# Kernel optimization log

Hardware: AMD Instinct MI355X
Metric: run time of the kernel (lower is better)

## Reference

```python
import jax, jax.numpy as jnp
import numpy as np

B, S, D, H = 4, 2048, 1024, 16
HD = D // H  # head dim = 64


def setup_inputs() -> dict:
    key = jax.random.key(0)
    ks = jax.random.split(key, 8)
    s = 1.0 / np.sqrt(D)
    return {
        "query": jax.random.normal(ks[0], (B, S, D), jnp.float32),
        "key": jax.random.normal(ks[1], (B, S, D), jnp.float32),
        "value": jax.random.normal(ks[2], (B, S, D), jnp.float32),
        "wq": jax.random.normal(ks[3], (D, D), jnp.float32) * s,
        "wk": jax.random.normal(ks[4], (D, D), jnp.float32) * s,
        "wv": jax.random.normal(ks[5], (D, D), jnp.float32) * s,
        "wo": jax.random.normal(ks[6], (D, D), jnp.float32) * s,
        "bo": jax.random.normal(ks[7], (D,), jnp.float32) * s,
    }


def reference(query, key, value, wq, wk, wv, wo, bo):
    # project and split heads: [B,S,D] -> [B,H,S,HD]
    def split_heads(x, w):
        return (x @ w.T).reshape(B, S, H, HD).transpose(0, 2, 1, 3)

    q = split_heads(query, wq)
    k = split_heads(key, wk)
    v = split_heads(value, wv)
    scores = jnp.einsum('bhqd,bhkd->bhqk', q, k) / jnp.sqrt(jnp.float32(HD))
    attn = jax.nn.softmax(scores, axis=-1)
    out = jnp.einsum('bhqk,bhkd->bhqd', attn, v)
    out = out.transpose(0, 2, 1, 3).reshape(B, S, D)
    return out @ wo.T + bo
```

## Files before the change

kernel.cpp:

```cpp
#include <hip/hip_runtime.h>
#include <stdint.h>


#define NSEQ 2048
#define NDIM 1024
#define NE   8388608

typedef unsigned short u16;
typedef unsigned int   u32;
typedef __bf16 bf16x8 __attribute__((ext_vector_type(8)));
typedef float  f32x4  __attribute__((ext_vector_type(4)));

__device__ __forceinline__ u16 f2bf(float f) {
  return (u16)((__builtin_bit_cast(u32, f) + 0x8000u) >> 16);
}
__device__ __forceinline__ u32 pack_bf2(float lo, float hi) {
  u32 a = __builtin_bit_cast(u32, lo) + 0x8000u;
  u32 b = __builtin_bit_cast(u32, hi) + 0x8000u;
  return __builtin_amdgcn_perm(b, a, 0x07060302);
}

__device__ __forceinline__ void async_load16(const u16* gsrc, u16* ldst) {
  __builtin_amdgcn_global_load_lds(
      (const __attribute__((address_space(1))) void*)gsrc,
      (__attribute__((address_space(3))) void*)ldst, 16, 0, 0);
}

__device__ __forceinline__ void conv_body(const float* __restrict__ src,
                                          u16* __restrict__ dst, int blk) {
  const int i = blk * 256 + (int)threadIdx.x;
  const float4 a = ((const float4*)src)[2 * i];
  const float4 b = ((const float4*)src)[2 * i + 1];
  uint4 o;
  o.x = pack_bf2(a.x, a.y); o.y = pack_bf2(a.z, a.w);
  o.z = pack_bf2(b.x, b.y); o.w = pack_bf2(b.z, b.w);
  ((uint4*)dst)[i] = o;
}
__global__ __launch_bounds__(256) void conv_big_kernel(
    const float* __restrict__ query, const float* __restrict__ keyi,
    const float* __restrict__ value, u16* __restrict__ Xq,
    u16* __restrict__ Xk, u16* __restrict__ Xv) {
  int blk = blockIdx.x;
  const float* src; u16* dst;
  if (blk < 4096)      { src = query; dst = Xq; }
  else if (blk < 8192) { src = keyi;  dst = Xk; blk -= 4096; }
  else                 { src = value; dst = Xv; blk -= 8192; }
  conv_body(src, dst, blk);
}
__global__ __launch_bounds__(256) void conv_w_kernel(
    const float* __restrict__ wq, const float* __restrict__ wk,
    const float* __restrict__ wv, const float* __restrict__ wo,
    u16* __restrict__ Wall) {
  int blk = blockIdx.x;
  const int z = blk >> 9;
  blk &= 511;
  const float* src = (z == 0) ? wq : (z == 1) ? wk : (z == 2) ? wv : wo;
  conv_body(src, Wall + (size_t)z * 1048576, blk);
}

template <bool OUTF32, bool BIAS>
__device__ __forceinline__ void gemm_core(const u16* __restrict__ A,
                                          const u16* __restrict__ B,
                                          void* __restrict__ Yv,
                                          const float* __restrict__ bias,
                                          float scale, long m0, long n0,
                                          long ldy) {
  __shared__ u16 At[128 * 32];
  __shared__ u16 Bt[128 * 32];
  const int t    = threadIdx.x;
  const int lane = t & 63;
  const int w    = t >> 6;
  const int m    = lane & 15;
  const int q    = lane >> 4;
  const int wr   = w >> 1;
  const int wc   = w & 1;
  const int srow = t >> 2;
  const int scol = (t & 3) * 8;

  f32x4 acc[4][4];
#pragma unroll
  for (int i = 0; i < 4; i++)
#pragma unroll
    for (int j = 0; j < 4; j++) acc[i][j] = (f32x4){0.f, 0.f, 0.f, 0.f};

  for (int k0 = 0; k0 < NDIM; k0 += 32) {
    __syncthreads();
    async_load16(A + (m0 + srow) * NDIM + k0 + scol, At + w * 512);
    async_load16(A + (m0 + 64 + srow) * NDIM + k0 + scol, At + 2048 + w * 512);
    async_load16(B + (n0 + srow) * NDIM + k0 + scol, Bt + w * 512);
    async_load16(B + (n0 + 64 + srow) * NDIM + k0 + scol, Bt + 2048 + w * 512);
    __syncthreads();

    bf16x8 a[4], b[4];
#pragma unroll
    for (int mi = 0; mi < 4; mi++)
      a[mi] = *(const bf16x8*)(At + (wr * 64 + mi * 16 + m) * 32 + q * 8);
#pragma unroll
    for (int ni = 0; ni < 4; ni++)
      b[ni] = *(const bf16x8*)(Bt + (wc * 64 + ni * 16 + m) * 32 + q * 8);
#pragma unroll
    for (int mi = 0; mi < 4; mi++)
#pragma unroll
      for (int ni = 0; ni < 4; ni++)
        acc[mi][ni] = __builtin_amdgcn_mfma_f32_16x16x32_bf16(a[mi], b[ni], acc[mi][ni], 0, 0, 0);
  }

#pragma unroll
  for (int mi = 0; mi < 4; mi++) {
#pragma unroll
    for (int ni = 0; ni < 4; ni++) {
      const long row0 = m0 + wr * 64 + mi * 16 + q * 4;
      const long col  = n0 + wc * 64 + ni * 16 + m;
      float badd = 0.f;
      if (BIAS) badd = bias[col];
#pragma unroll
      for (int r = 0; r < 4; r++) {
        const float v = acc[mi][ni][r] * scale + badd;
        if (OUTF32) ((float*)Yv)[(row0 + r) * ldy + col] = v;
        else        ((u16*)Yv)[(row0 + r) * ldy + col] = f2bf(v);
      }
    }
  }
}

__global__ __launch_bounds__(256) void gemm_qkv_kernel(
    const u16* __restrict__ Xq, const u16* __restrict__ Xk,
    const u16* __restrict__ Xv, const u16* __restrict__ Wall,
    u16* __restrict__ Qp, u16* __restrict__ Kp, u16* __restrict__ Vt) {
  const int z = blockIdx.z;
  if (z < 2) {
    const u16* A = z ? Xk : Xq;
    const u16* B = Wall + (size_t)z * 1048576;
    u16* Y       = z ? Kp : Qp;
    gemm_core<false, false>(A, B, Y, nullptr, z ? 1.0f : 0.18033688f,
                            (long)blockIdx.x * 128, (long)blockIdx.y * 128, NDIM);
  } else {
    const int flat = blockIdx.y * 64 + blockIdx.x;
    const long b   = flat >> 7;
    const int rem  = flat & 127;
    gemm_core<false, false>(Wall + 2 * 1048576, Xv + b * NSEQ * NDIM,
                            Vt + b * (long)NDIM * NSEQ, nullptr, 1.0f,
                            (long)(rem >> 4) * 128, (long)(rem & 15) * 128, NSEQ);
  }
}

__global__ __launch_bounds__(256) void gemm_out_kernel(
    const u16* __restrict__ A, const u16* __restrict__ Wall,
    float* __restrict__ Y, const float* __restrict__ bias) {
  gemm_core<true, true>(A, Wall + 3 * 1048576, Y, bias, 1.0f,
                        (long)blockIdx.x * 128, (long)blockIdx.y * 128, NDIM);
}

__global__ __launch_bounds__(256) void attn_kernel(
    const u16* __restrict__ Qp, const u16* __restrict__ Kp,
    const u16* __restrict__ Vtg, u16* __restrict__ Op) {
  __shared__ u16 Kt[64 * 72];
  __shared__ u16 Vt[64 * 72];
  __shared__ u16 Pt[4 * 32 * 72];
  const int t    = threadIdx.x;
  const int lane = t & 63;
  const int w    = t >> 6;
  const int m    = lane & 15;
  const int q    = lane >> 4;
  const int bh   = blockIdx.y;
  const int b    = bh >> 4;
  const int h    = bh & 15;
  const int wq0  = blockIdx.x * 128 + w * 32;
  const long base_bh = (long)b * NSEQ * NDIM + h * 64;
  const long vbase   = (long)b * NDIM * NSEQ + (long)(h * 64) * NSEQ;

  bf16x8 qf[2][2];
#pragma unroll
  for (int qi = 0; qi < 2; qi++)
#pragma unroll
    for (int ks = 0; ks < 2; ks++)
      qf[qi][ks] = *(const bf16x8*)(Qp + base_bh + (long)(wq0 + qi * 16 + m) * NDIM + ks * 32 + q * 8);

  f32x4 ot[2][4];
#pragma unroll
  for (int qi = 0; qi < 2; qi++)
#pragma unroll
    for (int mb = 0; mb < 4; mb++) ot[qi][mb] = (f32x4){0.f, 0.f, 0.f, 0.f};
  float lp[2] = {0.f, 0.f};

  const int srow = t >> 3;
  const int scol = (t & 7) * 8;
  u16* pt = Pt + w * (32 * 72);

  const u16* kgp = Kp + base_bh + (long)srow * NDIM + scol;
  const u16* vgp = Vtg + vbase + (long)srow * NSEQ + scol;

  int4 kr0 = *(const int4*)(kgp);
  int4 kr1 = *(const int4*)(kgp + 32l * NDIM);
  int4 vr0 = *(const int4*)(vgp);
  int4 vr1 = *(const int4*)(vgp + 32l * NSEQ);

  for (int kt = 0; kt < NSEQ / 64; kt++) {
    __syncthreads();
    *(int4*)(Kt + srow * 72 + scol)        = kr0;
    *(int4*)(Kt + (srow + 32) * 72 + scol) = kr1;
    *(int4*)(Vt + srow * 72 + scol)        = vr0;
    *(int4*)(Vt + (srow + 32) * 72 + scol) = vr1;
    __syncthreads();

    if (kt < NSEQ / 64 - 1) {
      const long k1 = (long)(kt + 1) * 64;
      kr0 = *(const int4*)(kgp + k1 * NDIM);
      kr1 = *(const int4*)(kgp + (k1 + 32) * NDIM);
      vr0 = *(const int4*)(vgp + k1);
      vr1 = *(const int4*)(vgp + 32l * NSEQ + k1);
    }

    f32x4 st[2][4];
#pragma unroll
    for (int qi = 0; qi < 2; qi++)
#pragma unroll
      for (int nb = 0; nb < 4; nb++) st[qi][nb] = (f32x4){0.f, 0.f, 0.f, 0.f};
    __builtin_amdgcn_s_setprio(1);
#pragma unroll
    for (int ks = 0; ks < 2; ks++) {
#pragma unroll
      for (int nb = 0; nb < 4; nb++) {
        bf16x8 kf = *(const bf16x8*)(Kt + (nb * 16 + m) * 72 + ks * 32 + q * 8);
        st[0][nb] = __builtin_amdgcn_mfma_f32_16x16x32_bf16(kf, qf[0][ks], st[0][nb], 0, 0, 0);
        st[1][nb] = __builtin_amdgcn_mfma_f32_16x16x32_bf16(kf, qf[1][ks], st[1][nb], 0, 0, 0);
      }
    }
    __builtin_amdgcn_s_setprio(0);

#pragma unroll
    for (int qi = 0; qi < 2; qi++)
#pragma unroll
      for (int nb = 0; nb < 4; nb++) {
        const float p0 = __builtin_amdgcn_exp2f(st[qi][nb][0]);
        const float p1 = __builtin_amdgcn_exp2f(st[qi][nb][1]);
        const float p2 = __builtin_amdgcn_exp2f(st[qi][nb][2]);
        const float p3 = __builtin_amdgcn_exp2f(st[qi][nb][3]);
        lp[qi] += (p0 + p1) + (p2 + p3);
        uint2 pk;
        pk.x = pack_bf2(p0, p1);
        pk.y = pack_bf2(p2, p3);
        *(uint2*)(pt + (qi * 16 + m) * 72 + nb * 16 + q * 4) = pk;
      }

    __builtin_amdgcn_s_setprio(1);
#pragma unroll
    for (int ks2 = 0; ks2 < 2; ks2++) {
      bf16x8 pf[2];
#pragma unroll
      for (int qi = 0; qi < 2; qi++)
        pf[qi] = *(const bf16x8*)(pt + (qi * 16 + m) * 72 + ks2 * 32 + q * 8);
#pragma unroll
      for (int mb = 0; mb < 4; mb++) {
        bf16x8 vf = *(const bf16x8*)(Vt + (mb * 16 + m) * 72 + ks2 * 32 + q * 8);
        ot[0][mb] = __builtin_amdgcn_mfma_f32_16x16x32_bf16(vf, pf[0], ot[0][mb], 0, 0, 0);
        ot[1][mb] = __builtin_amdgcn_mfma_f32_16x16x32_bf16(vf, pf[1], ot[1][mb], 0, 0, 0);
      }
    }
    __builtin_amdgcn_s_setprio(0);
  }

  float rinv[2];
#pragma unroll
  for (int qi = 0; qi < 2; qi++) {
    float v = lp[qi];
    v += __shfl_xor(v, 16);
    v += __shfl_xor(v, 32);
    rinv[qi] = 1.0f / v;
  }

#pragma unroll
  for (int qi = 0; qi < 2; qi++) {
#pragma unroll
    for (int mb = 0; mb < 4; mb++) {
      uint2 pk;
      pk.x = pack_bf2(ot[qi][mb][0] * rinv[qi], ot[qi][mb][1] * rinv[qi]);
      pk.y = pack_bf2(ot[qi][mb][2] * rinv[qi], ot[qi][mb][3] * rinv[qi]);
      *(uint2*)(pt + m * 72 + mb * 16 + q * 4) = pk;
    }
#pragma unroll
    for (int c = 0; c < 2; c++) {
      const int u   = c * 64 + lane;
      const int qr  = u >> 3;
      const int oct = u & 7;
      const int4 val = *(const int4*)(pt + qr * 72 + oct * 8);
      const long s   = wq0 + qi * 16 + qr;
      *(int4*)(Op + base_bh + s * NDIM + oct * 8) = val;
    }
  }
}

extern "C" void kernel_launch(void* const* d_in, const int* in_sizes, int n_in,
                              void* d_out, int out_size, void* d_ws, size_t ws_size,
                              hipStream_t stream) {
  const float* query = (const float*)d_in[0];
  const float* keyi  = (const float*)d_in[1];
  const float* value = (const float*)d_in[2];
  const float* wq    = (const float*)d_in[3];
  const float* wk    = (const float*)d_in[4];
  const float* wv    = (const float*)d_in[5];
  const float* wo    = (const float*)d_in[6];
  const float* bo    = (const float*)d_in[7];

  u16* ws = (u16*)d_ws;
  u16* Qp = ws;
  u16* Kp = ws + (size_t)NE;
  u16* Vt = ws + 2 * (size_t)NE;
  u16* XqO = ws + 3 * (size_t)NE;

  u16* Xk = (u16*)d_out;
  u16* Xv = (u16*)d_out + (size_t)NE;
  u16* Wall = (u16*)d_in[0];

  dim3 blk(256, 1, 1);
  conv_big_kernel<<<dim3(12288, 1, 1), blk, 0, stream>>>(query, keyi, value, XqO, Xk, Xv);
  conv_w_kernel<<<dim3(2048, 1, 1), blk, 0, stream>>>(wq, wk, wv, wo, Wall);
  gemm_qkv_kernel<<<dim3(64, 8, 3), blk, 0, stream>>>(XqO, Xk, Xv, Wall, Qp, Kp, Vt);
  attn_kernel<<<dim3(16, 64, 1), blk, 0, stream>>>(Qp, Kp, Vt, XqO);
  gemm_out_kernel<<<dim3(64, 8, 1), blk, 0, stream>>>(XqO, Wall, (float*)d_out, bo);
}
```

Before: 349.8 us.

## Keep softmax probabilities in registers by permuting V tile layout in LDS

The exp'd score fragments are packed directly into the B-operand registers of the PV MFMA instead of being written to and re-read from a per-wave LDS P buffer. To make that register layout line up, V columns are scattered into LDS with a permuted key ordering. The P shared buffer is removed, the epilogue reuses the K tile storage behind an extra barrier, and launch bounds request 4 blocks per CU to raise occupancy. The main risks are the correctness of the permutation and register pressure under the new launch bound.

```diff
diff --git a/kernel.cpp b/kernel.cpp
--- a/kernel.cpp
+++ b/kernel.cpp
@@ -151,12 +151,11 @@
                         (long)blockIdx.x * 128, (long)blockIdx.y * 128, NDIM);
 }
 
-__global__ __launch_bounds__(256) void attn_kernel(
+__global__ __launch_bounds__(256, 4) void attn_kernel(
     const u16* __restrict__ Qp, const u16* __restrict__ Kp,
     const u16* __restrict__ Vtg, u16* __restrict__ Op) {
   __shared__ u16 Kt[64 * 72];
   __shared__ u16 Vt[64 * 72];
-  __shared__ u16 Pt[4 * 32 * 72];
   const int t    = threadIdx.x;
   const int lane = t & 63;
   const int w    = t >> 6;
@@ -184,8 +183,13 @@
   float lp[2] = {0.f, 0.f};
 
   const int srow = t >> 3;
-  const int scol = (t & 7) * 8;
-  u16* pt = Pt + w * (32 * 72);
+  const int c8   = t & 7;
+  const int scol = c8 * 8;
+
+  const int vnb   = c8 >> 1;
+  const int vbase_c = 32 * (vnb >> 1) + 4 * (vnb & 1);
+  const int vcol0 = vbase_c + 8 * ((2 * c8) & 3);
+  const int vcol1 = vbase_c + 8 * ((2 * c8 + 1) & 3);
 
   const u16* kgp = Kp + base_bh + (long)srow * NDIM + scol;
   const u16* vgp = Vtg + vbase + (long)srow * NSEQ + scol;
@@ -195,12 +199,16 @@
   int4 vr0 = *(const int4*)(vgp);
   int4 vr1 = *(const int4*)(vgp + 32l * NSEQ);
 
+  const f32x4 zz = (f32x4){0.f, 0.f, 0.f, 0.f};
+
   for (int kt = 0; kt < NSEQ / 64; kt++) {
     __syncthreads();
     *(int4*)(Kt + srow * 72 + scol)        = kr0;
     *(int4*)(Kt + (srow + 32) * 72 + scol) = kr1;
-    *(int4*)(Vt + srow * 72 + scol)        = vr0;
-    *(int4*)(Vt + (srow + 32) * 72 + scol) = vr1;
+    *(uint2*)(Vt + srow * 72 + vcol0)        = make_uint2((u32)vr0.x, (u32)vr0.y);
+    *(uint2*)(Vt + srow * 72 + vcol1)        = make_uint2((u32)vr0.z, (u32)vr0.w);
+    *(uint2*)(Vt + (srow + 32) * 72 + vcol0) = make_uint2((u32)vr1.x, (u32)vr1.y);
+    *(uint2*)(Vt + (srow + 32) * 72 + vcol1) = make_uint2((u32)vr1.z, (u32)vr1.w);
     __syncthreads();
 
     if (kt < NSEQ / 64 - 1) {
@@ -212,22 +220,22 @@
     }
 
     f32x4 st[2][4];
-#pragma unroll
-    for (int qi = 0; qi < 2; qi++)
-#pragma unroll
-      for (int nb = 0; nb < 4; nb++) st[qi][nb] = (f32x4){0.f, 0.f, 0.f, 0.f};
     __builtin_amdgcn_s_setprio(1);
 #pragma unroll
-    for (int ks = 0; ks < 2; ks++) {
-#pragma unroll
-      for (int nb = 0; nb < 4; nb++) {
-        bf16x8 kf = *(const bf16x8*)(Kt + (nb * 16 + m) * 72 + ks * 32 + q * 8);
-        st[0][nb] = __builtin_amdgcn_mfma_f32_16x16x32_bf16(kf, qf[0][ks], st[0][nb], 0, 0, 0);
-        st[1][nb] = __builtin_amdgcn_mfma_f32_16x16x32_bf16(kf, qf[1][ks], st[1][nb], 0, 0, 0);
-      }
+    for (int nb = 0; nb < 4; nb++) {
+      bf16x8 kf = *(const bf16x8*)(Kt + (nb * 16 + m) * 72 + q * 8);
+      st[0][nb] = __builtin_amdgcn_mfma_f32_16x16x32_bf16(kf, qf[0][0], zz, 0, 0, 0);
+      st[1][nb] = __builtin_amdgcn_mfma_f32_16x16x32_bf16(kf, qf[1][0], zz, 0, 0, 0);
+    }
+#pragma unroll
+    for (int nb = 0; nb < 4; nb++) {
+      bf16x8 kf = *(const bf16x8*)(Kt + (nb * 16 + m) * 72 + 32 + q * 8);
+      st[0][nb] = __builtin_amdgcn_mfma_f32_16x16x32_bf16(kf, qf[0][1], st[0][nb], 0, 0, 0);
+      st[1][nb] = __builtin_amdgcn_mfma_f32_16x16x32_bf16(kf, qf[1][1], st[1][nb], 0, 0, 0);
     }
     __builtin_amdgcn_s_setprio(0);
 
+    u32 pkx[2][4], pky[2][4];
 #pragma unroll
     for (int qi = 0; qi < 2; qi++)
 #pragma unroll
@@ -237,10 +245,8 @@
         const float p2 = __builtin_amdgcn_exp2f(st[qi][nb][2]);
         const float p3 = __builtin_amdgcn_exp2f(st[qi][nb][3]);
         lp[qi] += (p0 + p1) + (p2 + p3);
-        uint2 pk;
-        pk.x = pack_bf2(p0, p1);
-        pk.y = pack_bf2(p2, p3);
-        *(uint2*)(pt + (qi * 16 + m) * 72 + nb * 16 + q * 4) = pk;
+        pkx[qi][nb] = pack_bf2(p0, p1);
+        pky[qi][nb] = pack_bf2(p2, p3);
       }
 
     __builtin_amdgcn_s_setprio(1);
@@ -248,8 +254,14 @@
     for (int ks2 = 0; ks2 < 2; ks2++) {
       bf16x8 pf[2];
 #pragma unroll
-      for (int qi = 0; qi < 2; qi++)
-        pf[qi] = *(const bf16x8*)(pt + (qi * 16 + m) * 72 + ks2 * 32 + q * 8);
+      for (int qi = 0; qi < 2; qi++) {
+        uint4 pw;
+        pw.x = pkx[qi][2 * ks2];
+        pw.y = pky[qi][2 * ks2];
+        pw.z = pkx[qi][2 * ks2 + 1];
+        pw.w = pky[qi][2 * ks2 + 1];
+        pf[qi] = __builtin_bit_cast(bf16x8, pw);
+      }
 #pragma unroll
       for (int mb = 0; mb < 4; mb++) {
         bf16x8 vf = *(const bf16x8*)(Vt + (mb * 16 + m) * 72 + ks2 * 32 + q * 8);
@@ -269,6 +281,8 @@
     rinv[qi] = 1.0f / v;
   }
 
+  __syncthreads();
+  u16* ept = Kt + w * 1152;
 #pragma unroll
   for (int qi = 0; qi < 2; qi++) {
 #pragma unroll
@@ -276,14 +290,14 @@
       uint2 pk;
       pk.x = pack_bf2(ot[qi][mb][0] * rinv[qi], ot[qi][mb][1] * rinv[qi]);
       pk.y = pack_bf2(ot[qi][mb][2] * rinv[qi], ot[qi][mb][3] * rinv[qi]);
-      *(uint2*)(pt + m * 72 + mb * 16 + q * 4) = pk;
+      *(uint2*)(ept + m * 72 + mb * 16 + q * 4) = pk;
     }
 #pragma unroll
     for (int c = 0; c < 2; c++) {
       const int u   = c * 64 + lane;
       const int qr  = u >> 3;
       const int oct = u & 7;
-      const int4 val = *(const int4*)(pt + qr * 72 + oct * 8);
+      const int4 val = *(const int4*)(ept + qr * 72 + oct * 8);
       const long s   = wq0 + qi * 16 + qr;
       *(int4*)(Op + base_bh + s * NDIM + oct * 8) = val;
     }
```

After: 337.2 us. 3.6% less time.
